# Optimization experiments

Measured on AMD Instinct MI355X. Metric: run time of the kernel, lower is better.

The kernel has to match this reference:

```python
import jax, jax.numpy as jnp
import numpy as np
from jax import lax

D_MODEL = 512
D_STATE = 16
D_CONV = 4
EXPAND = 2
D_INNER = EXPAND * D_MODEL          # 1024
DT_RANK = (D_MODEL + 15) // 16      # 32 (ceil(d_model/16))
BATCH = 8
SEQLEN = 2048


def _mamba_params(key):
    ks = jax.random.split(key, 6)
    s = 0.02
    return {
        'in_w':   jax.random.normal(ks[0], (2 * D_INNER, D_MODEL)) * s,
        'conv_w': jax.random.normal(ks[1], (D_INNER, D_CONV)) * s,
        'conv_b': jnp.zeros((D_INNER,)),
        'xp_w':   jax.random.normal(ks[2], (DT_RANK + 2 * D_STATE, D_INNER)) * s,
        'dt_w':   jax.random.normal(ks[3], (D_INNER, DT_RANK)) * s,
        'dt_b':   jax.random.uniform(ks[4], (D_INNER,), minval=-4.0, maxval=-2.0),
        'A_log':  jnp.log(jnp.tile(jnp.arange(1, D_STATE + 1, dtype=jnp.float32), (D_INNER, 1))),
        'Dp':     jnp.ones((D_INNER,)),
        'out_w':  jax.random.normal(ks[5], (D_MODEL, D_INNER)) * s,
    }


def setup_inputs() -> dict:
    key = jax.random.key(0)
    kx, kf, kb, kl1, kl2 = jax.random.split(key, 5)
    pf = _mamba_params(kf)
    pb = _mamba_params(kb)
    inp = {'x': jax.random.normal(kx, (BATCH, SEQLEN, D_MODEL), dtype=jnp.float32)}
    for name, v in pf.items():
        inp['f_' + name] = v
    for name, v in pb.items():
        inp['b_' + name] = v
    inp['lin_w'] = jax.random.normal(kl1, (D_MODEL, 2 * D_MODEL)) * 0.02
    inp['lin_b'] = jnp.zeros((D_MODEL,))
    return inp


def _mamba(x, in_w, conv_w, conv_b, xp_w, dt_w, dt_b, A_log, Dp, out_w):
    # x: (B, L, D_MODEL)
    Bsz = x.shape[0]
    xz = x @ in_w.T                                  # (B, L, 2*D_INNER)
    xi, z = jnp.split(xz, 2, axis=-1)
    # causal depthwise conv over time
    xc = jnp.transpose(xi, (0, 2, 1))                # (B, D_INNER, L)
    xc = lax.conv_general_dilated(
        xc, conv_w[:, None, :], (1,), [(D_CONV - 1, 0)],
        feature_group_count=D_INNER)
    xi = jax.nn.silu(jnp.transpose(xc + conv_b[None, :, None], (0, 2, 1)))
    # input-dependent SSM params
    dbl = xi @ xp_w.T                                # (B, L, DT_RANK + 2*N)
    dt = jax.nn.softplus(dbl[..., :DT_RANK] @ dt_w.T + dt_b)    # (B, L, D_INNER)
    Bm = dbl[..., DT_RANK:DT_RANK + D_STATE]                    # (B, L, N)
    Cm = dbl[..., DT_RANK + D_STATE:]                           # (B, L, N)
    A = -jnp.exp(A_log)                                         # (D_INNER, N)

    def step(h, inp):
        dt_t, B_t, C_t, x_t = inp                    # (B,Di), (B,N), (B,N), (B,Di)
        h = jnp.exp(dt_t[..., None] * A) * h + (dt_t * x_t)[..., None] * B_t[:, None, :]
        y = jnp.einsum('bdn,bn->bd', h, C_t)
        return h, y

    xs = (jnp.swapaxes(dt, 0, 1), jnp.swapaxes(Bm, 0, 1),
          jnp.swapaxes(Cm, 0, 1), jnp.swapaxes(xi, 0, 1))
    h0 = jnp.zeros((Bsz, D_INNER, D_STATE), dtype=x.dtype)
    _, ys = lax.scan(step, h0, xs)                   # ys: (L, B, D_INNER)
    y = jnp.swapaxes(ys, 0, 1) + xi * Dp
    y = y * jax.nn.silu(z)
    return y @ out_w.T                               # (B, L, D_MODEL)


def reference(x,
              f_in_w, f_conv_w, f_conv_b, f_xp_w, f_dt_w, f_dt_b, f_A_log, f_Dp, f_out_w,
              b_in_w, b_conv_w, b_conv_b, b_xp_w, b_dt_w, b_dt_b, b_A_log, b_Dp, b_out_w,
              lin_w, lin_b):
    y_fwd = _mamba(x, f_in_w, f_conv_w, f_conv_b, f_xp_w, f_dt_w, f_dt_b, f_A_log, f_Dp, f_out_w)
    y_bwd = _mamba(x[:, ::-1, :], b_in_w, b_conv_w, b_conv_b, b_xp_w, b_dt_w, b_dt_b,
                   b_A_log, b_Dp, b_out_w)[:, ::-1, :]
    y = jnp.concatenate([y_fwd, y_bwd], axis=-1)     # (B, L, 2*D_MODEL)
    return y @ lin_w.T + lin_b
```

## Files before the change

kernel.cpp:

```cpp
#include <hip/hip_runtime.h>
#include <cmath>

#define LSEQ 2048
#define NBATCH 8

typedef __attribute__((ext_vector_type(8))) short short8;
typedef __attribute__((ext_vector_type(4))) float f32x4;

__device__ __forceinline__ float silu_f(float x) { return x / (1.0f + __expf(-x)); }
__device__ __forceinline__ float softplus_f(float x) {
    return fmaxf(x, 0.0f) + log1pf(__expf(-fabsf(x)));
}
__device__ __forceinline__ unsigned short f2bf(float f) {
    unsigned int u = __float_as_uint(f);
    u += 0x7FFFu + ((u >> 16) & 1u);
    return (unsigned short)(u >> 16);
}
__device__ __forceinline__ float bf2f(unsigned short h) {
    return __uint_as_float(((unsigned int)h) << 16);
}
__device__ __forceinline__ void gload_lds16(const void* g, void* l) {
    __builtin_amdgcn_global_load_lds((const __attribute__((address_space(1))) void*)g,
                                     (__attribute__((address_space(3))) void*)l, 16, 0, 0);
}

#if defined(__has_builtin)
#if __has_builtin(__builtin_amdgcn_exp2f)
#define EXP2F(x) __builtin_amdgcn_exp2f(x)
#endif
#endif
#ifndef EXP2F
#define EXP2F(x) __expf((x) * 0.69314718055994531f)
#endif

struct GemmPair {
    const unsigned short* A[2];
    const unsigned short* A2[2];
    const unsigned short* W[2];
    const float* bias[2];
    void* C[2];
    unsigned short* aux[2];
};

template<int WGM, int WGN, int OMODE, int DK, int XTRA>
__global__ __launch_bounds__(WGM* WGN * 64) void gemm_mfma(GemmPair gp, int lda, int ldw,
                                                           int ldc, int K)
{
    constexpr int NW = WGM * WGN;
    constexpr int TM = WGM * 64, TN = WGN * 64;
    __shared__ unsigned short As[TM * 32];
    __shared__ unsigned short Bs[TN * 32];
    const int dir = blockIdx.z;
    const unsigned short* A  = gp.A[dir];
    const unsigned short* A2 = gp.A2[dir];
    const unsigned short* W  = gp.W[dir];
    const float* bias        = gp.bias[dir];
    void* Cout               = gp.C[dir];
    unsigned short* aux      = gp.aux[dir];

    const int tid = threadIdx.x;
    const int wave = tid >> 6, lane = tid & 63;
    const int wm = wave / WGN, wn = wave % WGN;
    const int m0 = blockIdx.x * TM, n0 = blockIdx.y * TN;
    const int l15 = lane & 15, l4 = lane >> 4;
    const int srow = lane >> 2, schunk = (lane & 3) * 8;

    f32x4 acc[4][4] = {};

    for (int k0 = 0; k0 < K; k0 += 32) {
        __syncthreads();
        for (int s = wave; s < TM / 16; s += NW) {
            const int gr = m0 + s * 16 + srow;
            const unsigned short* g;
            if (DK != 0 && k0 >= DK)
                g = A2 + (size_t)(gr ^ (LSEQ - 1)) * lda + (k0 - DK) + schunk;
            else
                g = A + (size_t)gr * lda + k0 + schunk;
            gload_lds16(g, (char*)As + (size_t)s * 1024);
        }
        for (int s = wave; s < TN / 16; s += NW) {
            const int gr = n0 + s * 16 + srow;
            const unsigned short* g = W + (size_t)gr * ldw + k0 + schunk;
            gload_lds16(g, (char*)Bs + (size_t)s * 1024);
        }
        __syncthreads();
        short8 af[4], bfr[4];
#pragma unroll
        for (int mi = 0; mi < 4; ++mi)
            af[mi] = *(const short8*)&As[(wm * 64 + mi * 16 + l15) * 32 + l4 * 8];
#pragma unroll
        for (int ni = 0; ni < 4; ++ni)
            bfr[ni] = *(const short8*)&Bs[(wn * 64 + ni * 16 + l15) * 32 + l4 * 8];
#pragma unroll
        for (int mi = 0; mi < 4; ++mi)
#pragma unroll
            for (int ni = 0; ni < 4; ++ni)
                acc[mi][ni] = __builtin_amdgcn_mfma_f32_16x16x32_bf16(af[mi], bfr[ni], acc[mi][ni], 0, 0, 0);
    }

#pragma unroll
    for (int mi = 0; mi < 4; ++mi)
#pragma unroll
        for (int ni = 0; ni < 4; ++ni)
#pragma unroll
            for (int r = 0; r < 4; ++r) {
                const int row = m0 + wm * 64 + mi * 16 + l4 * 4 + r;
                const int col = n0 + wn * 64 + ni * 16 + l15;
                float v = acc[mi][ni][r];
                if (bias) v += bias[col];
                if (OMODE & 1) ((unsigned short*)Cout)[(size_t)row * ldc + col] = f2bf(v);
                else           ((float*)Cout)[(size_t)row * ldc + col] = v;
                if (XTRA) { if (col < 32) aux[(size_t)row * 32 + col] = f2bf(v); }
            }
}

__global__ __launch_bounds__(256) void combine_k(
    const float* __restrict__ lin_w, const float* __restrict__ owf,
    const float* __restrict__ owb, unsigned short* __restrict__ Wcomb)
{
    const int dir = blockIdx.z;
    const float* ow = dir ? owb : owf;
    const int lane = threadIdx.x & 63;
    const int wave = threadIdx.x >> 6;
    const int n = blockIdx.y * 4 + wave;
    const int d = blockIdx.x * 256 + lane * 4;
    float4 acc = {0.f, 0.f, 0.f, 0.f};
    const float* lrow = lin_w + (size_t)n * 1024 + dir * 512;
    for (int j = 0; j < 512; ++j) {
        const float s = lrow[j];
        const float4 v = *(const float4*)&ow[(size_t)j * 1024 + d];
        acc.x = fmaf(s, v.x, acc.x); acc.y = fmaf(s, v.y, acc.y);
        acc.z = fmaf(s, v.z, acc.z); acc.w = fmaf(s, v.w, acc.w);
    }
    ushort4 o;
    o.x = f2bf(acc.x); o.y = f2bf(acc.y); o.z = f2bf(acc.z); o.w = f2bf(acc.w);
    *(ushort4*)&Wcomb[(size_t)n * 2048 + dir * 1024 + d] = o;
}

struct CvtArgs { const float* s[6]; unsigned short* d[6]; int n[6]; };
__global__ __launch_bounds__(256) void cvt_k(CvtArgs a)
{
    const int sid = blockIdx.y;
    const float* s = a.s[sid];
    unsigned short* d = a.d[sid];
    const int n4 = a.n[sid] >> 2;
    for (int i = blockIdx.x * 256 + threadIdx.x; i < n4; i += gridDim.x * 256) {
        const float4 v = ((const float4*)s)[i];
        ushort4 o; o.x = f2bf(v.x); o.y = f2bf(v.y); o.z = f2bf(v.z); o.w = f2bf(v.w);
        ((ushort4*)d)[i] = o;
    }
}
__global__ __launch_bounds__(256) void cvtx_k(const float* __restrict__ s,
                                              unsigned short* __restrict__ d, int n4)
{
    for (int i = blockIdx.x * 256 + threadIdx.x; i < n4; i += gridDim.x * 256) {
        const float4 v = ((const float4*)s)[i];
        ushort4 o; o.x = f2bf(v.x); o.y = f2bf(v.y); o.z = f2bf(v.z); o.w = f2bf(v.w);
        ((ushort4*)d)[i] = o;
    }
}

__global__ __launch_bounds__(256) void conv_silu_k(
    const unsigned short* __restrict__ xz_f, const float* __restrict__ cw_f,
    const float* __restrict__ cb_f, unsigned short* __restrict__ xi_f,
    const unsigned short* __restrict__ xz_b, const float* __restrict__ cw_b,
    const float* __restrict__ cb_b, unsigned short* __restrict__ xi_b)
{
    const int dir = blockIdx.y;
    const unsigned short* xz = dir ? xz_b : xz_f;
    const float* cw = dir ? cw_b : cw_f;
    const float* cb = dir ? cb_b : cb_f;
    unsigned short* xi = dir ? xi_b : xi_f;

    const int bt = blockIdx.x;
    const int b = bt >> 11;
    const int t = bt & (LSEQ - 1);
    const int d = threadIdx.x << 2;

    float w[4][4];
#pragma unroll
    for (int i = 0; i < 4; ++i) {
        const float4 wr = *(const float4*)&cw[(d + i) * 4];
        w[i][0] = wr.x; w[i][1] = wr.y; w[i][2] = wr.z; w[i][3] = wr.w;
    }
    float4 acc = *(const float4*)&cb[d];
#pragma unroll
    for (int k = 0; k < 4; ++k) {
        const int row = dir ? (LSEQ - 1 - t) + 3 - k : t - 3 + k;
        if ((unsigned)row < (unsigned)LSEQ) {
            const ushort4 v = *(const ushort4*)&xz[(size_t)(b * LSEQ + row) * 2048 + d];
            acc.x += w[0][k] * bf2f(v.x); acc.y += w[1][k] * bf2f(v.y);
            acc.z += w[2][k] * bf2f(v.z); acc.w += w[3][k] * bf2f(v.w);
        }
    }
    ushort4 st;
    st.x = f2bf(silu_f(acc.x)); st.y = f2bf(silu_f(acc.y));
    st.z = f2bf(silu_f(acc.z)); st.w = f2bf(silu_f(acc.w));
    *(ushort4*)&xi[(size_t)(b * LSEQ + t) * 1024 + d] = st;
}

__device__ __forceinline__ float row_sum8(float x) {
    x += __int_as_float(__builtin_amdgcn_update_dpp(0, __float_as_int(x), 0xB1, 0xF, 0xF, false));
    x += __int_as_float(__builtin_amdgcn_update_dpp(0, __float_as_int(x), 0x4E, 0xF, 0xF, false));
    x += __int_as_float(__builtin_amdgcn_update_dpp(0, __float_as_int(x), 0x141, 0xF, 0xF, false));
    return x;
}

struct ScanPair {
    const unsigned short* dblh[2];
    const unsigned short* dtw[2];
    const float* dtb[2];
    unsigned short* xiy[2];
    const float* dbl[2];
    const unsigned short* xz[2];
    const float* Al[2];
    const float* Dp[2];
};

__global__ __launch_bounds__(256) void scan_k(ScanPair sp)
{
    __shared__ float sdt[32][68], sdtx[32][68], sxi[32][68];
    __shared__ float sB2[8][140], sC2[8][140];
    __shared__ float sy[64][36];

    const int dir = blockIdx.z;
    const unsigned short* dblh = sp.dblh[dir];
    const unsigned short* dtw  = sp.dtw[dir];
    const float* dtb           = sp.dtb[dir];
    unsigned short* xiy        = sp.xiy[dir];
    const float* dbl           = sp.dbl[dir];
    const unsigned short* zz   = sp.xz[dir];
    const float* Al            = sp.Al[dir];
    const float* Dpp           = sp.Dp[dir];

    const int b = blockIdx.y, d0 = blockIdx.x << 5;
    const int tid = threadIdx.x;
    const int wave = tid >> 6, lane = tid & 63;
    const int l15 = lane & 15, l4 = lane >> 4;
    const int di = tid >> 3, np = tid & 7;
    const int lr = tid >> 2, lc = tid & 3;

    const float A0L = -expf(Al[(d0 + di) * 16 + np]) * 1.4426950408889634f;
    const float A1L = -expf(Al[(d0 + di) * 16 + np + 8]) * 1.4426950408889634f;

    const short8 dtwf0 = *(const short8*)&dtw[(size_t)(d0 + l15) * 32 + l4 * 8];
    const short8 dtwf1 = *(const short8*)&dtw[(size_t)(d0 + 16 + l15) * 32 + l4 * 8];
    const float dtb0 = dtb[d0 + l15], dtb1 = dtb[d0 + 16 + l15];

    float dpv[8];
#pragma unroll
    for (int i = 0; i < 8; ++i) dpv[i] = Dpp[d0 + lc * 8 + i];

    ushort4 pxi0, pxi1;
    float4 pB, pC;
    short8 pA;
    auto issue_loads = [&](int c) {
        const size_t r = (size_t)b * LSEQ + c * 64 + lr;
        pxi0 = *(const ushort4*)&xiy[r * 1024 + d0 + lc * 8];
        pxi1 = *(const ushort4*)&xiy[r * 1024 + d0 + lc * 8 + 4];
        pB   = *(const float4*)&dbl[r * 64 + 32 + lc * 4];
        pC   = *(const float4*)&dbl[r * 64 + 48 + lc * 4];
        pA   = *(const short8*)&dblh[(size_t)(b * LSEQ + c * 64 + wave * 16 + l15) * 32 + l4 * 8];
    };
    issue_loads(0);

    float h0 = 0.0f, h1 = 0.0f;
    for (int c = 0; c < LSEQ / 64; ++c) {
        const int t0 = c * 64;
        __syncthreads();
        sxi[lc * 8 + 0][lr] = bf2f(pxi0.x);
        sxi[lc * 8 + 1][lr] = bf2f(pxi0.y);
        sxi[lc * 8 + 2][lr] = bf2f(pxi0.z);
        sxi[lc * 8 + 3][lr] = bf2f(pxi0.w);
        sxi[lc * 8 + 4][lr] = bf2f(pxi1.x);
        sxi[lc * 8 + 5][lr] = bf2f(pxi1.y);
        sxi[lc * 8 + 6][lr] = bf2f(pxi1.z);
        sxi[lc * 8 + 7][lr] = bf2f(pxi1.w);
        {
            const float bv[4] = {pB.x, pB.y, pB.z, pB.w};
            const float cv[4] = {pC.x, pC.y, pC.z, pC.w};
#pragma unroll
            for (int i = 0; i < 4; ++i) {
                const int n = lc * 4 + i;
                sB2[n & 7][lr * 2 + (n >> 3)] = bv[i];
                sC2[n & 7][lr * 2 + (n >> 3)] = cv[i];
            }
        }
        __syncthreads();
        {
            f32x4 z4 = {0.f, 0.f, 0.f, 0.f};
            f32x4 dacc0 = __builtin_amdgcn_mfma_f32_16x16x32_bf16(pA, dtwf0, z4, 0, 0, 0);
            f32x4 dacc1 = __builtin_amdgcn_mfma_f32_16x16x32_bf16(pA, dtwf1, z4, 0, 0, 0);
            const int tq = wave * 16 + l4 * 4;
            const float4 xi0 = *(const float4*)&sxi[l15][tq];
            const float4 xi1 = *(const float4*)&sxi[16 + l15][tq];
            float4 dv0, dv1, dx0, dx1;
            dv0.x = softplus_f(dacc0[0] + dtb0); dv0.y = softplus_f(dacc0[1] + dtb0);
            dv0.z = softplus_f(dacc0[2] + dtb0); dv0.w = softplus_f(dacc0[3] + dtb0);
            dv1.x = softplus_f(dacc1[0] + dtb1); dv1.y = softplus_f(dacc1[1] + dtb1);
            dv1.z = softplus_f(dacc1[2] + dtb1); dv1.w = softplus_f(dacc1[3] + dtb1);
            dx0.x = dv0.x * xi0.x; dx0.y = dv0.y * xi0.y;
            dx0.z = dv0.z * xi0.z; dx0.w = dv0.w * xi0.w;
            dx1.x = dv1.x * xi1.x; dx1.y = dv1.y * xi1.y;
            dx1.z = dv1.z * xi1.z; dx1.w = dv1.w * xi1.w;
            *(float4*)&sdt[l15][tq]       = dv0;
            *(float4*)&sdt[16 + l15][tq]  = dv1;
            *(float4*)&sdtx[l15][tq]      = dx0;
            *(float4*)&sdtx[16 + l15][tq] = dx1;
        }
        if (c + 1 < LSEQ / 64) issue_loads(c + 1);
        ushort4 pz0, pz1;
        {
            const int tz = dir ? (LSEQ - 1 - (t0 + lr)) : (t0 + lr);
            pz0 = *(const ushort4*)&zz[((size_t)b * LSEQ + tz) * 2048 + 1024 + d0 + lc * 8];
            pz1 = *(const ushort4*)&zz[((size_t)b * LSEQ + tz) * 2048 + 1024 + d0 + lc * 8 + 4];
        }
        __syncthreads();
#pragma unroll 4
        for (int tt = 0; tt < 64; tt += 4) {
            const float4 d4 = *(const float4*)&sdt[di][tt];
            const float4 u4 = *(const float4*)&sdtx[di][tt];
            const float4 bA = *(const float4*)&sB2[np][tt * 2];
            const float4 bB = *(const float4*)&sB2[np][tt * 2 + 4];
            const float4 cA = *(const float4*)&sC2[np][tt * 2];
            const float4 cB = *(const float4*)&sC2[np][tt * 2 + 4];
            {
                h0 = fmaf(EXP2F(d4.x * A0L), h0, u4.x * bA.x);
                h1 = fmaf(EXP2F(d4.x * A1L), h1, u4.x * bA.y);
                const float pp = row_sum8(fmaf(h1, cA.y, h0 * cA.x));
                if (np == 0) sy[tt + 0][di] = pp;
            }
            {
                h0 = fmaf(EXP2F(d4.y * A0L), h0, u4.y * bA.z);
                h1 = fmaf(EXP2F(d4.y * A1L), h1, u4.y * bA.w);
                const float pp = row_sum8(fmaf(h1, cA.w, h0 * cA.z));
                if (np == 0) sy[tt + 1][di] = pp;
            }
            {
                h0 = fmaf(EXP2F(d4.z * A0L), h0, u4.z * bB.x);
                h1 = fmaf(EXP2F(d4.z * A1L), h1, u4.z * bB.y);
                const float pp = row_sum8(fmaf(h1, cB.y, h0 * cB.x));
                if (np == 0) sy[tt + 2][di] = pp;
            }
            {
                h0 = fmaf(EXP2F(d4.w * A0L), h0, u4.w * bB.z);
                h1 = fmaf(EXP2F(d4.w * A1L), h1, u4.w * bB.w);
                const float pp = row_sum8(fmaf(h1, cB.w, h0 * cB.z));
                if (np == 0) sy[tt + 3][di] = pp;
            }
        }
        __syncthreads();
        {
            const size_t r = (size_t)b * LSEQ + t0 + lr;
            const float4 y0 = *(const float4*)&sy[lr][lc * 8];
            const float4 y1 = *(const float4*)&sy[lr][lc * 8 + 4];
            float xiv[8];
#pragma unroll
            for (int i = 0; i < 8; ++i) xiv[i] = sxi[lc * 8 + i][lr];
            ushort4 s0, s1;
            s0.x = f2bf(fmaf(xiv[0], dpv[0], y0.x) * silu_f(bf2f(pz0.x)));
            s0.y = f2bf(fmaf(xiv[1], dpv[1], y0.y) * silu_f(bf2f(pz0.y)));
            s0.z = f2bf(fmaf(xiv[2], dpv[2], y0.z) * silu_f(bf2f(pz0.z)));
            s0.w = f2bf(fmaf(xiv[3], dpv[3], y0.w) * silu_f(bf2f(pz0.w)));
            s1.x = f2bf(fmaf(xiv[4], dpv[4], y1.x) * silu_f(bf2f(pz1.x)));
            s1.y = f2bf(fmaf(xiv[5], dpv[5], y1.y) * silu_f(bf2f(pz1.y)));
            s1.z = f2bf(fmaf(xiv[6], dpv[6], y1.z) * silu_f(bf2f(pz1.z)));
            s1.w = f2bf(fmaf(xiv[7], dpv[7], y1.w) * silu_f(bf2f(pz1.w)));
            *(ushort4*)&xiy[r * 1024 + d0 + lc * 8] = s0;
            *(ushort4*)&xiy[r * 1024 + d0 + lc * 8 + 4] = s1;
        }
    }
}

extern "C" void kernel_launch(void* const* d_in, const int* in_sizes, int n_in,
                              void* d_out, int out_size, void* d_ws, size_t ws_size,
                              hipStream_t stream)
{
    const float* x      = (const float*)d_in[0];
    const float* f_in_w = (const float*)d_in[1];
    const float* f_cw   = (const float*)d_in[2];
    const float* f_cb   = (const float*)d_in[3];
    const float* f_xp   = (const float*)d_in[4];
    const float* f_dtw  = (const float*)d_in[5];
    const float* f_dtb  = (const float*)d_in[6];
    const float* f_Al   = (const float*)d_in[7];
    const float* f_Dp   = (const float*)d_in[8];
    const float* f_ow   = (const float*)d_in[9];
    const float* b_in_w = (const float*)d_in[10];
    const float* b_cw   = (const float*)d_in[11];
    const float* b_cb   = (const float*)d_in[12];
    const float* b_xp   = (const float*)d_in[13];
    const float* b_dtw  = (const float*)d_in[14];
    const float* b_dtb  = (const float*)d_in[15];
    const float* b_Al   = (const float*)d_in[16];
    const float* b_Dp   = (const float*)d_in[17];
    const float* b_ow   = (const float*)d_in[18];
    const float* lin_w  = (const float*)d_in[19];
    const float* lin_b  = (const float*)d_in[20];
    float* out = (float*)d_out;

    char* p = (char*)d_ws;
    auto take = [&](size_t bytes) -> char* {
        char* r = p; p += (bytes + 255) & ~(size_t)255; return r;
    };

    unsigned short* wif  = (unsigned short*)take((size_t)2048 * 512 * 2);
    unsigned short* wib  = (unsigned short*)take((size_t)2048 * 512 * 2);
    unsigned short* wxf  = (unsigned short*)take((size_t)64 * 1024 * 2);
    unsigned short* wxb  = (unsigned short*)take((size_t)64 * 1024 * 2);
    unsigned short* wdtf = (unsigned short*)take((size_t)1024 * 32 * 2);
    unsigned short* wdtb = (unsigned short*)take((size_t)1024 * 32 * 2);
    unsigned short* wcmb = (unsigned short*)take((size_t)512 * 2048 * 2);

    const size_t used = (size_t)(p - (char*)d_ws);
    const size_t perRow = 1024 + 2 * (4096 + 2048 + 256 + 64);
    int G = 1;
    for (int g = 8; g >= 1; g >>= 1) {
        const size_t need = used + (size_t)g * LSEQ * perRow + 16384;
        if (need <= ws_size || g == 1) { G = g; break; }
    }

    CvtArgs ca;
    ca.s[0] = f_in_w; ca.d[0] = wif;  ca.n[0] = 2048 * 512;
    ca.s[1] = b_in_w; ca.d[1] = wib;  ca.n[1] = 2048 * 512;
    ca.s[2] = f_xp;   ca.d[2] = wxf;  ca.n[2] = 64 * 1024;
    ca.s[3] = b_xp;   ca.d[3] = wxb;  ca.n[3] = 64 * 1024;
    ca.s[4] = f_dtw;  ca.d[4] = wdtf; ca.n[4] = 1024 * 32;
    ca.s[5] = b_dtw;  ca.d[5] = wdtb; ca.n[5] = 1024 * 32;
    cvt_k<<<dim3(128, 6), 256, 0, stream>>>(ca);

    combine_k<<<dim3(4, 128, 2), 256, 0, stream>>>(lin_w, f_ow, b_ow, wcmb);

    char* pg0 = p;
    for (int g0 = 0; g0 < NBATCH; g0 += G) {
        const int Mg = G * LSEQ;
        p = pg0;
        unsigned short* xbf   = (unsigned short*)take((size_t)Mg * 512 * 2);
        unsigned short* xz_f  = (unsigned short*)take((size_t)Mg * 2048 * 2);
        unsigned short* xz_b  = (unsigned short*)take((size_t)Mg * 2048 * 2);
        unsigned short* xiy_f = (unsigned short*)take((size_t)Mg * 1024 * 2);
        unsigned short* xiy_b = (unsigned short*)take((size_t)Mg * 1024 * 2);
        float* dbl_f          = (float*)take((size_t)Mg * 64 * 4);
        float* dbl_b          = (float*)take((size_t)Mg * 64 * 4);
        unsigned short* dblh_f= (unsigned short*)take((size_t)Mg * 32 * 2);
        unsigned short* dblh_b= (unsigned short*)take((size_t)Mg * 32 * 2);

        const float* xg = x + (size_t)g0 * LSEQ * 512;
        float* outg = out + (size_t)g0 * LSEQ * 512;

        cvtx_k<<<dim3(512), 256, 0, stream>>>(xg, xbf, Mg * 512 / 4);

        GemmPair g1 = {};
        g1.A[0] = xbf; g1.A[1] = xbf; g1.W[0] = wif; g1.W[1] = wib;
        g1.C[0] = xz_f; g1.C[1] = xz_b;
        gemm_mfma<2,2,1,0,0><<<dim3(Mg/128, 16, 2), 256, 0, stream>>>(g1, 512, 512, 2048, 512);

        conv_silu_k<<<dim3(Mg, 2), 256, 0, stream>>>(xz_f, f_cw, f_cb, xiy_f,
                                                     xz_b, b_cw, b_cb, xiy_b);

        GemmPair g2 = {};
        g2.A[0] = xiy_f; g2.A[1] = xiy_b; g2.W[0] = wxf; g2.W[1] = wxb;
        g2.C[0] = dbl_f; g2.C[1] = dbl_b; g2.aux[0] = dblh_f; g2.aux[1] = dblh_b;
        gemm_mfma<4,1,0,0,1><<<dim3(Mg/256, 1, 2), 256, 0, stream>>>(g2, 1024, 1024, 64, 1024);

        ScanPair spp = {};
        spp.dblh[0] = dblh_f; spp.dblh[1] = dblh_b;
        spp.dtw[0] = wdtf;    spp.dtw[1] = wdtb;
        spp.dtb[0] = f_dtb;   spp.dtb[1] = b_dtb;
        spp.xiy[0] = xiy_f;   spp.xiy[1] = xiy_b;
        spp.dbl[0] = dbl_f;   spp.dbl[1] = dbl_b;
        spp.xz[0] = xz_f;     spp.xz[1] = xz_b;
        spp.Al[0] = f_Al;     spp.Al[1] = b_Al;
        spp.Dp[0] = f_Dp;     spp.Dp[1] = b_Dp;
        scan_k<<<dim3(32, G, 2), 256, 0, stream>>>(spp);

        GemmPair g5 = {};
        g5.A[0] = xiy_f; g5.A2[0] = xiy_b; g5.W[0] = wcmb;
        g5.bias[0] = lin_b; g5.C[0] = outg;
        gemm_mfma<2,2,0,1024,0><<<dim3(Mg/128, 4, 1), 256, 0, stream>>>(g5, 1024, 2048, 512, 2048);
    }
}
```

Baseline: 812.1 us.

## Double-buffer xi in LDS to drop a barrier, batch y stores, cheaper activations

Makes the xi shared-memory tile double-buffered and transposes it to a [t][d] layout, which removes the leading __syncthreads in each chunk of the scan loop. Lead lanes now store scan outputs as one float4 per four timesteps instead of four scalar stores, with the sy layout transposed to match. Silu uses a hardware reciprocal, softplus uses the fast __logf instead of log1pf, DPP bound_ctrl is set, and launch bounds request two blocks per CU. The trade-offs are extra LDS, strided scalar LDS reads in two places, and slightly lower activation precision.

```diff
diff --git a/kernel.cpp b/kernel.cpp
--- a/kernel.cpp
+++ b/kernel.cpp
@@ -7,9 +7,11 @@
 typedef __attribute__((ext_vector_type(8))) short short8;
 typedef __attribute__((ext_vector_type(4))) float f32x4;
 
-__device__ __forceinline__ float silu_f(float x) { return x / (1.0f + __expf(-x)); }
+__device__ __forceinline__ float silu_f(float x) {
+    return x * __builtin_amdgcn_rcpf(1.0f + __expf(-x));
+}
 __device__ __forceinline__ float softplus_f(float x) {
-    return fmaxf(x, 0.0f) + log1pf(__expf(-fabsf(x)));
+    return fmaxf(x, 0.0f) + __logf(1.0f + __expf(-fabsf(x)));
 }
 __device__ __forceinline__ unsigned short f2bf(float f) {
     unsigned int u = __float_as_uint(f);
@@ -200,9 +202,9 @@
 }
 
 __device__ __forceinline__ float row_sum8(float x) {
-    x += __int_as_float(__builtin_amdgcn_update_dpp(0, __float_as_int(x), 0xB1, 0xF, 0xF, false));
-    x += __int_as_float(__builtin_amdgcn_update_dpp(0, __float_as_int(x), 0x4E, 0xF, 0xF, false));
-    x += __int_as_float(__builtin_amdgcn_update_dpp(0, __float_as_int(x), 0x141, 0xF, 0xF, false));
+    x += __int_as_float(__builtin_amdgcn_update_dpp(0, __float_as_int(x), 0xB1, 0xF, 0xF, true));
+    x += __int_as_float(__builtin_amdgcn_update_dpp(0, __float_as_int(x), 0x4E, 0xF, 0xF, true));
+    x += __int_as_float(__builtin_amdgcn_update_dpp(0, __float_as_int(x), 0x141, 0xF, 0xF, true));
     return x;
 }
 
@@ -217,11 +219,12 @@
     const float* Dp[2];
 };
 
-__global__ __launch_bounds__(256) void scan_k(ScanPair sp)
-{
-    __shared__ float sdt[32][68], sdtx[32][68], sxi[32][68];
+__global__ __launch_bounds__(256, 2) void scan_k(ScanPair sp)
+{
+    __shared__ float sxi[2][64][36];
+    __shared__ float sdt[32][68], sdtx[32][68];
     __shared__ float sB2[8][140], sC2[8][140];
-    __shared__ float sy[64][36];
+    __shared__ float sy[32][68];
 
     const int dir = blockIdx.z;
     const unsigned short* dblh = sp.dblh[dir];
@@ -239,6 +242,7 @@
     const int l15 = lane & 15, l4 = lane >> 4;
     const int di = tid >> 3, np = tid & 7;
     const int lr = tid >> 2, lc = tid & 3;
+    const bool lead = (np == 0);
 
     const float A0L = -expf(Al[(d0 + di) * 16 + np]) * 1.4426950408889634f;
     const float A1L = -expf(Al[(d0 + di) * 16 + np + 8]) * 1.4426950408889634f;
@@ -267,15 +271,14 @@
     float h0 = 0.0f, h1 = 0.0f;
     for (int c = 0; c < LSEQ / 64; ++c) {
         const int t0 = c * 64;
-        __syncthreads();
-        sxi[lc * 8 + 0][lr] = bf2f(pxi0.x);
-        sxi[lc * 8 + 1][lr] = bf2f(pxi0.y);
-        sxi[lc * 8 + 2][lr] = bf2f(pxi0.z);
-        sxi[lc * 8 + 3][lr] = bf2f(pxi0.w);
-        sxi[lc * 8 + 4][lr] = bf2f(pxi1.x);
-        sxi[lc * 8 + 5][lr] = bf2f(pxi1.y);
-        sxi[lc * 8 + 6][lr] = bf2f(pxi1.z);
-        sxi[lc * 8 + 7][lr] = bf2f(pxi1.w);
+        const int buf = c & 1;
+        {
+            float4 xa, xb;
+            xa.x = bf2f(pxi0.x); xa.y = bf2f(pxi0.y); xa.z = bf2f(pxi0.z); xa.w = bf2f(pxi0.w);
+            xb.x = bf2f(pxi1.x); xb.y = bf2f(pxi1.y); xb.z = bf2f(pxi1.z); xb.w = bf2f(pxi1.w);
+            *(float4*)&sxi[buf][lr][lc * 8]     = xa;
+            *(float4*)&sxi[buf][lr][lc * 8 + 4] = xb;
+        }
         {
             const float bv[4] = {pB.x, pB.y, pB.z, pB.w};
             const float cv[4] = {pC.x, pC.y, pC.z, pC.w};
@@ -292,8 +295,11 @@
             f32x4 dacc0 = __builtin_amdgcn_mfma_f32_16x16x32_bf16(pA, dtwf0, z4, 0, 0, 0);
             f32x4 dacc1 = __builtin_amdgcn_mfma_f32_16x16x32_bf16(pA, dtwf1, z4, 0, 0, 0);
             const int tq = wave * 16 + l4 * 4;
-            const float4 xi0 = *(const float4*)&sxi[l15][tq];
-            const float4 xi1 = *(const float4*)&sxi[16 + l15][tq];
+            float4 xi0, xi1;
+            xi0.x = sxi[buf][tq + 0][l15];      xi0.y = sxi[buf][tq + 1][l15];
+            xi0.z = sxi[buf][tq + 2][l15];      xi0.w = sxi[buf][tq + 3][l15];
+            xi1.x = sxi[buf][tq + 0][16 + l15]; xi1.y = sxi[buf][tq + 1][16 + l15];
+            xi1.z = sxi[buf][tq + 2][16 + l15]; xi1.w = sxi[buf][tq + 3][16 + l15];
             float4 dv0, dv1, dx0, dx1;
             dv0.x = softplus_f(dacc0[0] + dtb0); dv0.y = softplus_f(dacc0[1] + dtb0);
             dv0.z = softplus_f(dacc0[2] + dtb0); dv0.w = softplus_f(dacc0[3] + dtb0);
@@ -324,48 +330,38 @@
             const float4 bB = *(const float4*)&sB2[np][tt * 2 + 4];
             const float4 cA = *(const float4*)&sC2[np][tt * 2];
             const float4 cB = *(const float4*)&sC2[np][tt * 2 + 4];
-            {
-                h0 = fmaf(EXP2F(d4.x * A0L), h0, u4.x * bA.x);
-                h1 = fmaf(EXP2F(d4.x * A1L), h1, u4.x * bA.y);
-                const float pp = row_sum8(fmaf(h1, cA.y, h0 * cA.x));
-                if (np == 0) sy[tt + 0][di] = pp;
-            }
-            {
-                h0 = fmaf(EXP2F(d4.y * A0L), h0, u4.y * bA.z);
-                h1 = fmaf(EXP2F(d4.y * A1L), h1, u4.y * bA.w);
-                const float pp = row_sum8(fmaf(h1, cA.w, h0 * cA.z));
-                if (np == 0) sy[tt + 1][di] = pp;
-            }
-            {
-                h0 = fmaf(EXP2F(d4.z * A0L), h0, u4.z * bB.x);
-                h1 = fmaf(EXP2F(d4.z * A1L), h1, u4.z * bB.y);
-                const float pp = row_sum8(fmaf(h1, cB.y, h0 * cB.x));
-                if (np == 0) sy[tt + 2][di] = pp;
-            }
-            {
-                h0 = fmaf(EXP2F(d4.w * A0L), h0, u4.w * bB.z);
-                h1 = fmaf(EXP2F(d4.w * A1L), h1, u4.w * bB.w);
-                const float pp = row_sum8(fmaf(h1, cB.w, h0 * cB.z));
-                if (np == 0) sy[tt + 3][di] = pp;
-            }
+            float4 ppv;
+            h0 = fmaf(EXP2F(d4.x * A0L), h0, u4.x * bA.x);
+            h1 = fmaf(EXP2F(d4.x * A1L), h1, u4.x * bA.y);
+            ppv.x = row_sum8(fmaf(h1, cA.y, h0 * cA.x));
+            h0 = fmaf(EXP2F(d4.y * A0L), h0, u4.y * bA.z);
+            h1 = fmaf(EXP2F(d4.y * A1L), h1, u4.y * bA.w);
+            ppv.y = row_sum8(fmaf(h1, cA.w, h0 * cA.z));
+            h0 = fmaf(EXP2F(d4.z * A0L), h0, u4.z * bB.x);
+            h1 = fmaf(EXP2F(d4.z * A1L), h1, u4.z * bB.y);
+            ppv.z = row_sum8(fmaf(h1, cB.y, h0 * cB.x));
+            h0 = fmaf(EXP2F(d4.w * A0L), h0, u4.w * bB.z);
+            h1 = fmaf(EXP2F(d4.w * A1L), h1, u4.w * bB.w);
+            ppv.w = row_sum8(fmaf(h1, cB.w, h0 * cB.z));
+            if (lead) *(float4*)&sy[di][tt] = ppv;
         }
         __syncthreads();
         {
             const size_t r = (size_t)b * LSEQ + t0 + lr;
-            const float4 y0 = *(const float4*)&sy[lr][lc * 8];
-            const float4 y1 = *(const float4*)&sy[lr][lc * 8 + 4];
-            float xiv[8];
-#pragma unroll
-            for (int i = 0; i < 8; ++i) xiv[i] = sxi[lc * 8 + i][lr];
+            const float4 xa = *(const float4*)&sxi[buf][lr][lc * 8];
+            const float4 xb = *(const float4*)&sxi[buf][lr][lc * 8 + 4];
+            float yv[8];
+#pragma unroll
+            for (int i = 0; i < 8; ++i) yv[i] = sy[lc * 8 + i][lr];
             ushort4 s0, s1;
-            s0.x = f2bf(fmaf(xiv[0], dpv[0], y0.x) * silu_f(bf2f(pz0.x)));
-            s0.y = f2bf(fmaf(xiv[1], dpv[1], y0.y) * silu_f(bf2f(pz0.y)));
-            s0.z = f2bf(fmaf(xiv[2], dpv[2], y0.z) * silu_f(bf2f(pz0.z)));
-            s0.w = f2bf(fmaf(xiv[3], dpv[3], y0.w) * silu_f(bf2f(pz0.w)));
-            s1.x = f2bf(fmaf(xiv[4], dpv[4], y1.x) * silu_f(bf2f(pz1.x)));
-            s1.y = f2bf(fmaf(xiv[5], dpv[5], y1.y) * silu_f(bf2f(pz1.y)));
-            s1.z = f2bf(fmaf(xiv[6], dpv[6], y1.z) * silu_f(bf2f(pz1.z)));
-            s1.w = f2bf(fmaf(xiv[7], dpv[7], y1.w) * silu_f(bf2f(pz1.w)));
+            s0.x = f2bf(fmaf(xa.x, dpv[0], yv[0]) * silu_f(bf2f(pz0.x)));
+            s0.y = f2bf(fmaf(xa.y, dpv[1], yv[1]) * silu_f(bf2f(pz0.y)));
+            s0.z = f2bf(fmaf(xa.z, dpv[2], yv[2]) * silu_f(bf2f(pz0.z)));
+            s0.w = f2bf(fmaf(xa.w, dpv[3], yv[3]) * silu_f(bf2f(pz0.w)));
+            s1.x = f2bf(fmaf(xb.x, dpv[4], yv[4]) * silu_f(bf2f(pz1.x)));
+            s1.y = f2bf(fmaf(xb.y, dpv[5], yv[5]) * silu_f(bf2f(pz1.y)));
+            s1.z = f2bf(fmaf(xb.z, dpv[6], yv[6]) * silu_f(bf2f(pz1.z)));
+            s1.w = f2bf(fmaf(xb.w, dpv[7], yv[7]) * silu_f(bf2f(pz1.w)));
             *(ushort4*)&xiy[r * 1024 + d0 + lc * 8] = s0;
             *(ushort4*)&xiy[r * 1024 + d0 + lc * 8 + 4] = s1;
         }
```

After: 736.9 us. 9.3% less time.
